# Optimization experiments

Measured on AMD Instinct MI355X. Metric: run time of the kernel, lower is better.

The kernel has to match this reference:

```python
import jax, jax.numpy as jnp
import numpy as np

HEADS = 4
C = 128            # per-head out channels (hard-coded 128 in the module)
NEG_SLOPE_ATT = 0.2   # GATConv attention leaky_relu slope
NEG_SLOPE = 0.01      # F.leaky_relu default slope


def _diag_output_ids(num_groups, n):
    # ids = base_i + n*j + j for group i, agent j; base_i = i * n^2
    i = np.arange(num_groups)[:, None] * (n * n)
    j = np.arange(n)[None, :] * (n + 1)
    return jnp.asarray((i + j).reshape(-1))


def setup_inputs() -> dict:
    key = jax.random.key(0)
    ks = jax.random.split(key, 12)
    num_groups, n_agents = 12, 48
    N = num_groups * n_agents * n_agents      # 27648 nodes
    E = 442368
    F_in, edge_dim, hidden = 256, 16, 256
    s = 0.05
    return {
        "x": jax.random.normal(ks[0], (N, F_in), jnp.float32),
        "edge_index": jax.random.randint(ks[1], (2, E), 0, N, jnp.int32),
        "edge_attr": jax.random.normal(ks[2], (E, edge_dim), jnp.float32),
        "num_groups": num_groups,
        "agents_per_group": n_agents,
        "W": jax.random.normal(ks[3], (F_in, HEADS * C), jnp.float32) * s,
        "att_src": jax.random.normal(ks[4], (HEADS, C), jnp.float32) * s,
        "att_dst": jax.random.normal(ks[5], (HEADS, C), jnp.float32) * s,
        "W_edge": jax.random.normal(ks[6], (edge_dim, HEADS * C), jnp.float32) * s,
        "att_edge": jax.random.normal(ks[7], (HEADS, C), jnp.float32) * s,
        "bias_gat": jnp.zeros((HEADS * C,), jnp.float32),
        "fc_W": jax.random.normal(ks[8], (HEADS * C, hidden), jnp.float32) * s,
        "fc_b": jnp.zeros((hidden,), jnp.float32),
    }


def _gat_conv(x, src, dst, edge_attr_full, W, att_src, att_dst, W_edge, att_edge, bias):
    N = x.shape[0]
    h = (x @ W).reshape(N, HEADS, C)                       # [N,H,C]
    a_src = jnp.einsum('nhc,hc->nh', h, att_src)           # [N,H]
    a_dst = jnp.einsum('nhc,hc->nh', h, att_dst)
    he = (edge_attr_full @ W_edge).reshape(-1, HEADS, C)   # [E',H,C]
    a_edge = jnp.einsum('ehc,hc->eh', he, att_edge)
    logits = jax.nn.leaky_relu(a_src[src] + a_dst[dst] + a_edge, NEG_SLOPE_ATT)
    # segment softmax over incoming edges of each dst node
    m = jax.ops.segment_max(logits, dst, num_segments=N)   # [N,H]
    e = jnp.exp(logits - m[dst])
    s = jax.ops.segment_sum(e, dst, num_segments=N)
    alpha = e / (s[dst] + 1e-16)                           # [E',H]
    msg = h[src] * alpha[..., None]                        # [E',H,C]
    out = jax.ops.segment_sum(msg, dst, num_segments=N)    # [N,H,C]
    return out.reshape(N, HEADS * C) + bias


def reference(x, edge_index, edge_attr, num_groups, agents_per_group,
              W, att_src, att_dst, W_edge, att_edge, bias_gat, fc_W, fc_b):
    N = x.shape[0]
    # add self-loops (PyG default), self-loop edge_attr = mean fill
    loops = jnp.arange(N, dtype=edge_index.dtype)
    src = jnp.concatenate([edge_index[0], loops])
    dst = jnp.concatenate([edge_index[1], loops])
    ea = jnp.concatenate([edge_attr,
                          jnp.broadcast_to(edge_attr.mean(0), (N, edge_attr.shape[1]))])
    h = jax.nn.leaky_relu(
        _gat_conv(x, src, dst, ea, W, att_src, att_dst, W_edge, att_edge, bias_gat),
        NEG_SLOPE)
    ids = _diag_output_ids(num_groups, agents_per_group)
    # fc_output + leaky_relu then diagonal index-select (select first: same math)
    return jax.nn.leaky_relu(h[ids] @ fc_W + fc_b, NEG_SLOPE)
```

## Files before the change

### kernel.cpp

```cpp
#include <hip/hip_runtime.h>

#define NNODES 27648
#define NEDGES 442368
#define FIN    256
#define HC     512
#define NH     4
#define CDIM   128
#define NAG    48
#define NGRP   12
#define N2     2304
#define NOUT   576
#define CAP    128
#define EDIM   16
#define MPART  512


__device__ __forceinline__ float lrelu(float v, float s){ return v > 0.0f ? v : s * v; }

__device__ __forceinline__ float wsum(float v){
  #pragma unroll
  for (int off = 32; off; off >>= 1) v += __shfl_xor(v, off, 64);
  return v;
}
__device__ __forceinline__ float wmax(float v){
  #pragma unroll
  for (int off = 32; off; off >>= 1) v = fmaxf(v, __shfl_xor(v, off, 64));
  return v;
}

__global__ __launch_bounds__(256) void k_pre(
    const float* __restrict__ W, const float* __restrict__ att_src,
    const float* __restrict__ att_dst, const float* __restrict__ W_edge,
    const float* __restrict__ att_edge, const float* __restrict__ ea,
    float* __restrict__ ws_, float* __restrict__ wd_, float* __restrict__ we_,
    int* __restrict__ counts, float4* __restrict__ easum_part){
  int b = blockIdx.x;
  int tid = threadIdx.x;
  if (b < 11) {
    int g = b * 256 + tid;
    if (g < 1024) {
      int f = g >> 2, h = g & 3;
      const float4* wp = (const float4*)(W + f*HC + h*CDIM);
      const float4* ap = (const float4*)(att_src + h*CDIM);
      float s = 0.f;
      #pragma unroll 8
      for (int c4 = 0; c4 < CDIM/4; c4++){
        float4 wv = wp[c4], av = ap[c4];
        s += wv.x*av.x + wv.y*av.y + wv.z*av.z + wv.w*av.w;
      }
      ws_[g] = s;
    } else if (g < 2048) {
      int gg = g - 1024; int f = gg >> 2, h = gg & 3;
      const float4* wp = (const float4*)(W + f*HC + h*CDIM);
      const float4* ap = (const float4*)(att_dst + h*CDIM);
      float s = 0.f;
      #pragma unroll 8
      for (int c4 = 0; c4 < CDIM/4; c4++){
        float4 wv = wp[c4], av = ap[c4];
        s += wv.x*av.x + wv.y*av.y + wv.z*av.z + wv.w*av.w;
      }
      wd_[gg] = s;
    } else if (g < 2112) {
      int gg = g - 2048; int d = gg >> 2, h = gg & 3;
      const float4* wp = (const float4*)(W_edge + d*HC + h*CDIM);
      const float4* ap = (const float4*)(att_edge + h*CDIM);
      float s = 0.f;
      #pragma unroll 8
      for (int c4 = 0; c4 < CDIM/4; c4++){
        float4 wv = wp[c4], av = ap[c4];
        s += wv.x*av.x + wv.y*av.y + wv.z*av.z + wv.w*av.w;
      }
      we_[gg] = s;
    } else if (g < 2112 + NOUT) {
      counts[g - 2112] = 0;
    }
  } else {
    int pb = b - 11;
    const float4* p = (const float4*)ea;
    const int total = NEDGES * 4;
    float4 acc = make_float4(0.f, 0.f, 0.f, 0.f);
    for (int i = pb*256 + tid; i < total; i += MPART*256){
      float4 v = p[i];
      acc.x += v.x; acc.y += v.y; acc.z += v.z; acc.w += v.w;
    }
    #pragma unroll
    for (int off = 4; off <= 32; off <<= 1){
      acc.x += __shfl_xor(acc.x, off, 64);
      acc.y += __shfl_xor(acc.y, off, 64);
      acc.z += __shfl_xor(acc.z, off, 64);
      acc.w += __shfl_xor(acc.w, off, 64);
    }
    __shared__ float4 sd4[16];
    int lane = tid & 63, wave = tid >> 6;
    if (lane < 4) sd4[wave*4 + lane] = acc;
    __syncthreads();
    if (tid < 4){
      float4 t = sd4[tid];
      float4 a = sd4[4+tid], c = sd4[8+tid], d = sd4[12+tid];
      t.x += a.x + c.x + d.x; t.y += a.y + c.y + d.y;
      t.z += a.z + c.z + d.z; t.w += a.w + c.w + d.w;
      easum_part[pb*4 + tid] = t;
    }
  }
}

__global__ __launch_bounds__(256) void k_scan(const int* __restrict__ ei,
    const float* __restrict__ ea, const float* __restrict__ we_,
    int* __restrict__ counts, int* __restrict__ slist, float* __restrict__ aed,
    const float* __restrict__ easum_part, float* __restrict__ easum){
  int tid = threadIdx.x;
  if (blockIdx.x == NEDGES/256){
    int col = tid & 15, part = tid >> 4;
    float s = 0.f;
    for (int pb = 0; pb < MPART/16; pb++)
      s += easum_part[(part*(MPART/16) + pb)*16 + col];
    __shared__ float sd[256];
    sd[tid] = s;
    __syncthreads();
    if (tid < 16){
      float t = 0.f;
      #pragma unroll
      for (int i = 0; i < 16; i++) t += sd[i*16 + tid];
      easum[tid] = t;
    }
    return;
  }
  int e = blockIdx.x*256 + tid;
  int dst = ei[NEDGES + e];
  int r = dst % N2;
  if (r % 49) return;
  int row = (dst / N2) * NAG + r / 49;
  int pos = atomicAdd(&counts[row], 1);
  if (pos >= CAP) return;
  slist[row*CAP + pos] = ei[e];
  const float* eap = ea + (size_t)e*EDIM;
  float a0=0.f,a1=0.f,a2=0.f,a3=0.f;
  #pragma unroll
  for (int d = 0; d < EDIM; d++){
    float v = eap[d];
    a0 += v*we_[d*4+0]; a1 += v*we_[d*4+1]; a2 += v*we_[d*4+2]; a3 += v*we_[d*4+3];
  }
  float* ap = aed + (size_t)(row*CAP+pos)*4;
  ap[0]=a0; ap[1]=a1; ap[2]=a2; ap[3]=a3;
}

__global__ __launch_bounds__(256) void k_mega(const float* __restrict__ x,
    const float* __restrict__ ws_, const float* __restrict__ wd_,
    const float* __restrict__ we_, const float* __restrict__ easum,
    const int* __restrict__ counts, const int* __restrict__ slist,
    const float* __restrict__ aed,
    const float* __restrict__ W, const float* __restrict__ bias,
    const float* __restrict__ fcW, const float* __restrict__ fcb,
    float* __restrict__ out){
  __shared__ float  lg[(CAP+1)*4];
  __shared__ int    srcs[CAP+1];
  __shared__ float  adst_s[4];
  __shared__ float4 pz4[4*256];
  __shared__ float4 zs4[256];
  __shared__ float4 ph4[256];
  __shared__ float  hs[512];
  __shared__ float4 pq4[256];
  int row = blockIdx.x;
  int g = row / NAG, j = row - g*NAG;
  int dst = g*N2 + j*49;
  int tid = threadIdx.x;
  int lane = tid & 63, wave = tid >> 6;
  int k = counts[row]; if (k > CAP) k = CAP;

  float wsr[4][4];
  #pragma unroll
  for (int q = 0; q < 4; q++){
    float4 t = *(const float4*)(ws_ + (lane*4+q)*4);
    wsr[q][0]=t.x; wsr[q][1]=t.y; wsr[q][2]=t.z; wsr[q][3]=t.w;
  }

  for (int i = wave; i < k; i += 4){
    int src = slist[row*CAP + i];
    float4 aedv = *(const float4*)(aed + (size_t)(row*CAP+i)*4);
    float4 xv = *(const float4*)(x + (size_t)src*FIN + lane*4);
    float p0 = xv.x*wsr[0][0] + xv.y*wsr[1][0] + xv.z*wsr[2][0] + xv.w*wsr[3][0];
    float p1 = xv.x*wsr[0][1] + xv.y*wsr[1][1] + xv.z*wsr[2][1] + xv.w*wsr[3][1];
    float p2 = xv.x*wsr[0][2] + xv.y*wsr[1][2] + xv.z*wsr[2][2] + xv.w*wsr[3][2];
    float p3 = xv.x*wsr[0][3] + xv.y*wsr[1][3] + xv.z*wsr[2][3] + xv.w*wsr[3][3];
    p0 = wsum(p0); p1 = wsum(p1); p2 = wsum(p2); p3 = wsum(p3);
    if (lane == 0){
      srcs[i] = src;
      lg[i*4+0] = p0 + aedv.x; lg[i*4+1] = p1 + aedv.y;
      lg[i*4+2] = p2 + aedv.z; lg[i*4+3] = p3 + aedv.w;
    }
  }

  if (wave == 0){
    float wdr[4][4];
    #pragma unroll
    for (int q = 0; q < 4; q++){
      float4 t = *(const float4*)(wd_ + (lane*4+q)*4);
      wdr[q][0]=t.x; wdr[q][1]=t.y; wdr[q][2]=t.z; wdr[q][3]=t.w;
    }
    float4 xv = *(const float4*)(x + (size_t)dst*FIN + lane*4);
    float pd[4], ps[4];
    #pragma unroll
    for (int h = 0; h < 4; h++){
      pd[h] = xv.x*wdr[0][h] + xv.y*wdr[1][h] + xv.z*wdr[2][h] + xv.w*wdr[3][h];
      ps[h] = xv.x*wsr[0][h] + xv.y*wsr[1][h] + xv.z*wsr[2][h] + xv.w*wsr[3][h];
    }
    const float invE = 1.0f/(float)NEDGES;
    float md = (lane < 16) ? easum[lane]*invE : 0.f;
    float al[4];
    #pragma unroll
    for (int h = 0; h < 4; h++){
      float c = (lane < 16) ? md*we_[lane*4+h] : 0.f;
      al[h] = wsum(c);
      pd[h] = wsum(pd[h]);
      ps[h] = wsum(ps[h]);
    }
    if (lane == 0){
      #pragma unroll
      for (int h = 0; h < 4; h++){
        adst_s[h] = pd[h];
        lg[k*4+h] = ps[h] + al[h];
      }
      srcs[k] = dst;
    }
  }
  __syncthreads();

  {
    int h = wave;
    float ad = adst_s[h];
    float m = -1e30f;
    for (int i = lane; i <= k; i += 64){
      float v = lrelu(lg[i*4+h] + ad, 0.2f);
      lg[i*4+h] = v;
      m = fmaxf(m, v);
    }
    m = wmax(m);
    float s = 0.f;
    for (int i = lane; i <= k; i += 64){
      float e = __expf(lg[i*4+h] - m);
      lg[i*4+h] = e;
      s += e;
    }
    s = wsum(s);
    float inv = 1.0f/(s + 1e-16f);
    for (int i = lane; i <= k; i += 64) lg[i*4+h] *= inv;
  }
  __syncthreads();

  {
    float acc[4][4];
    #pragma unroll
    for (int h = 0; h < 4; h++)
      #pragma unroll
      for (int c = 0; c < 4; c++) acc[h][c] = 0.f;
    for (int i = wave; i <= k; i += 4){
      int src = srcs[i];
      float4 xv = *(const float4*)(x + (size_t)src*FIN + lane*4);
      float a0 = lg[i*4+0], a1 = lg[i*4+1], a2 = lg[i*4+2], a3 = lg[i*4+3];
      acc[0][0] += a0*xv.x; acc[0][1] += a0*xv.y; acc[0][2] += a0*xv.z; acc[0][3] += a0*xv.w;
      acc[1][0] += a1*xv.x; acc[1][1] += a1*xv.y; acc[1][2] += a1*xv.z; acc[1][3] += a1*xv.w;
      acc[2][0] += a2*xv.x; acc[2][1] += a2*xv.y; acc[2][2] += a2*xv.z; acc[2][3] += a2*xv.w;
      acc[3][0] += a3*xv.x; acc[3][1] += a3*xv.y; acc[3][2] += a3*xv.z; acc[3][3] += a3*xv.w;
    }
    #pragma unroll
    for (int h = 0; h < 4; h++)
      pz4[wave*256 + h*64 + lane] =
        make_float4(acc[h][0], acc[h][1], acc[h][2], acc[h][3]);
  }
  __syncthreads();
  {
    float4 a = pz4[0*256+tid], b = pz4[1*256+tid],
           c = pz4[2*256+tid], d = pz4[3*256+tid];
    zs4[tid] = make_float4(a.x+b.x+c.x+d.x, a.y+b.y+c.y+d.y,
                           a.z+b.z+c.z+d.z, a.w+b.w+c.w+d.w);
  }
  __syncthreads();

  {
    int cg = tid & 127;
    int half = tid >> 7;
    int h = cg >> 5;
    const float* zp = (const float*)zs4 + h*256 + half*128;
    const float4* Wp = (const float4*)(W + (size_t)half*128*HC) + cg;
    float4 acc = make_float4(0.f,0.f,0.f,0.f);
    #pragma unroll 8
    for (int r = 0; r < 128; r++){
      float4 w4 = Wp[(size_t)r*(HC/4)];
      float zv = zp[r];
      acc.x += zv*w4.x; acc.y += zv*w4.y; acc.z += zv*w4.z; acc.w += zv*w4.w;
    }
    ph4[half*128 + cg] = acc;
  }
  __syncthreads();
  if (tid < 128){
    float4 a = ph4[tid], b = ph4[128+tid];
    float4 bs = *(const float4*)(bias + 4*tid);
    hs[4*tid+0] = lrelu(a.x+b.x+bs.x, 0.01f);
    hs[4*tid+1] = lrelu(a.y+b.y+bs.y, 0.01f);
    hs[4*tid+2] = lrelu(a.z+b.z+bs.z, 0.01f);
    hs[4*tid+3] = lrelu(a.w+b.w+bs.w, 0.01f);
  }
  __syncthreads();

  {
    int cg = tid & 63;
    int q  = tid >> 6;
    const float4* Fp = (const float4*)(fcW + (size_t)q*128*256) + cg;
    const float* hp = hs + q*128;
    float4 acc = make_float4(0.f,0.f,0.f,0.f);
    #pragma unroll 8
    for (int r = 0; r < 128; r++){
      float4 w4 = Fp[(size_t)r*64];
      float hv = hp[r];
      acc.x += hv*w4.x; acc.y += hv*w4.y; acc.z += hv*w4.z; acc.w += hv*w4.w;
    }
    pq4[q*64 + cg] = acc;
  }
  __syncthreads();
  if (tid < 64){
    float4 a = pq4[tid],      b = pq4[64+tid];
    float4 c = pq4[128+tid],  d = pq4[192+tid];
    float4 bs = *(const float4*)(fcb + 4*tid);
    float4 o;
    o.x = lrelu(a.x+b.x+c.x+d.x+bs.x, 0.01f);
    o.y = lrelu(a.y+b.y+c.y+d.y+bs.y, 0.01f);
    o.z = lrelu(a.z+b.z+c.z+d.z+bs.z, 0.01f);
    o.w = lrelu(a.w+b.w+c.w+d.w+bs.w, 0.01f);
    *(float4*)(out + (size_t)row*256 + 4*tid) = o;
  }
}

extern "C" void kernel_launch(void* const* d_in, const int* in_sizes, int n_in,
                              void* d_out, int out_size, void* d_ws, size_t ws_size,
                              hipStream_t stream) {
  const float* x        = (const float*)d_in[0];
  const int*   ei       = (const int*)  d_in[1];
  const float* ea       = (const float*)d_in[2];
  const float* W        = (const float*)d_in[5];
  const float* att_src  = (const float*)d_in[6];
  const float* att_dst  = (const float*)d_in[7];
  const float* W_edge   = (const float*)d_in[8];
  const float* att_edge = (const float*)d_in[9];
  const float* bias     = (const float*)d_in[10];
  const float* fcW      = (const float*)d_in[11];
  const float* fcb      = (const float*)d_in[12];
  float* out = (float*)d_out;

  float* w = (float*)d_ws;
  float*  ws_       = w;
  float*  wd_       = w + 1024;
  float*  we_       = w + 2048;
  float*  easum     = w + 2112;
  int*    counts    = (int*)(w + 2128);
  float*  easum_p   = w + 2704;
  int*    slist     = (int*)(w + 10896);
  float*  aed       = w + 84624;

  k_pre<<<11 + MPART, 256, 0, stream>>>(W, att_src, att_dst, W_edge, att_edge, ea,
                                        ws_, wd_, we_, counts, (float4*)easum_p);
  k_scan<<<NEDGES/256 + 1, 256, 0, stream>>>(ei, ea, we_, counts, slist, aed,
                                             easum_p, easum);
  k_mega<<<NOUT, 256, 0, stream>>>(x, ws_, wd_, we_, easum, counts, slist, aed,
                                   W, bias, fcW, fcb, out);
}
```

Before: 156.6 us.

## Process two output rows per block to share W and fc weight loads

k_mega now handles two destination rows per 512-thread block, with each group of four waves doing gather and softmax for one row. The two dense projections (W and fc_W) are split over more K-slices, and each weight load feeds both rows' accumulators, which halves the global weight traffic per row. The cost is half as many blocks (288), which may underfill the GPU, plus larger shared memory use and an extra reduction step.

```diff
diff --git a/kernel.cpp b/kernel.cpp
--- a/kernel.cpp
+++ b/kernel.cpp
@@ -144,7 +144,7 @@
   ap[0]=a0; ap[1]=a1; ap[2]=a2; ap[3]=a3;
 }
 
-__global__ __launch_bounds__(256) void k_mega(const float* __restrict__ x,
+__global__ __launch_bounds__(512) void k_mega(const float* __restrict__ x,
     const float* __restrict__ ws_, const float* __restrict__ wd_,
     const float* __restrict__ we_, const float* __restrict__ easum,
     const int* __restrict__ counts, const int* __restrict__ slist,
@@ -152,20 +152,24 @@
     const float* __restrict__ W, const float* __restrict__ bias,
     const float* __restrict__ fcW, const float* __restrict__ fcb,
     float* __restrict__ out){
-  __shared__ float  lg[(CAP+1)*4];
-  __shared__ int    srcs[CAP+1];
-  __shared__ float  adst_s[4];
-  __shared__ float4 pz4[4*256];
-  __shared__ float4 zs4[256];
-  __shared__ float4 ph4[256];
-  __shared__ float  hs[512];
-  __shared__ float4 pq4[256];
-  int row = blockIdx.x;
-  int g = row / NAG, j = row - g*NAG;
-  int dst = g*N2 + j*49;
+  __shared__ float  lg[2][(CAP+1)*4];
+  __shared__ int    srcs[2][CAP+1];
+  __shared__ float  adst[2][4];
+  __shared__ float4 zs4[2][256];
+  __shared__ float  hsf[2][512];
+  __shared__ float4 scratch[2048];
+  int rowA = blockIdx.x * 2;
   int tid = threadIdx.x;
   int lane = tid & 63, wave = tid >> 6;
-  int k = counts[row]; if (k > CAP) k = CAP;
+  int rsel = wave >> 2;
+  int w4 = wave & 3;
+
+  int kA = counts[rowA];     if (kA > CAP) kA = CAP;
+  int kB = counts[rowA + 1]; if (kB > CAP) kB = CAP;
+  int myRow = rowA + rsel;
+  int myK = rsel ? kB : kA;
+  int gg = myRow / NAG, jj = myRow - gg*NAG;
+  int myDst = gg*N2 + jj*49;
 
   float wsr[4][4];
   #pragma unroll
@@ -174,9 +178,9 @@
     wsr[q][0]=t.x; wsr[q][1]=t.y; wsr[q][2]=t.z; wsr[q][3]=t.w;
   }
 
-  for (int i = wave; i < k; i += 4){
-    int src = slist[row*CAP + i];
-    float4 aedv = *(const float4*)(aed + (size_t)(row*CAP+i)*4);
+  for (int i = w4; i < myK; i += 4){
+    int src = slist[myRow*CAP + i];
+    float4 aedv = *(const float4*)(aed + (size_t)(myRow*CAP+i)*4);
     float4 xv = *(const float4*)(x + (size_t)src*FIN + lane*4);
     float p0 = xv.x*wsr[0][0] + xv.y*wsr[1][0] + xv.z*wsr[2][0] + xv.w*wsr[3][0];
     float p1 = xv.x*wsr[0][1] + xv.y*wsr[1][1] + xv.z*wsr[2][1] + xv.w*wsr[3][1];
@@ -184,20 +188,20 @@
     float p3 = xv.x*wsr[0][3] + xv.y*wsr[1][3] + xv.z*wsr[2][3] + xv.w*wsr[3][3];
     p0 = wsum(p0); p1 = wsum(p1); p2 = wsum(p2); p3 = wsum(p3);
     if (lane == 0){
-      srcs[i] = src;
-      lg[i*4+0] = p0 + aedv.x; lg[i*4+1] = p1 + aedv.y;
-      lg[i*4+2] = p2 + aedv.z; lg[i*4+3] = p3 + aedv.w;
-    }
-  }
-
-  if (wave == 0){
+      srcs[rsel][i] = src;
+      lg[rsel][i*4+0] = p0 + aedv.x; lg[rsel][i*4+1] = p1 + aedv.y;
+      lg[rsel][i*4+2] = p2 + aedv.z; lg[rsel][i*4+3] = p3 + aedv.w;
+    }
+  }
+
+  if (w4 == 0){
     float wdr[4][4];
     #pragma unroll
     for (int q = 0; q < 4; q++){
       float4 t = *(const float4*)(wd_ + (lane*4+q)*4);
       wdr[q][0]=t.x; wdr[q][1]=t.y; wdr[q][2]=t.z; wdr[q][3]=t.w;
     }
-    float4 xv = *(const float4*)(x + (size_t)dst*FIN + lane*4);
+    float4 xv = *(const float4*)(x + (size_t)myDst*FIN + lane*4);
     float pd[4], ps[4];
     #pragma unroll
     for (int h = 0; h < 4; h++){
@@ -217,33 +221,34 @@
     if (lane == 0){
       #pragma unroll
       for (int h = 0; h < 4; h++){
-        adst_s[h] = pd[h];
-        lg[k*4+h] = ps[h] + al[h];
+        adst[rsel][h] = pd[h];
+        lg[rsel][myK*4+h] = ps[h] + al[h];
       }
-      srcs[k] = dst;
-    }
-  }
-  __syncthreads();
-
-  {
-    int h = wave;
-    float ad = adst_s[h];
+      srcs[rsel][myK] = myDst;
+    }
+  }
+  __syncthreads();
+
+  {
+    int r = wave >> 2, h = wave & 3;
+    int kk = r ? kB : kA;
+    float ad = adst[r][h];
     float m = -1e30f;
-    for (int i = lane; i <= k; i += 64){
-      float v = lrelu(lg[i*4+h] + ad, 0.2f);
-      lg[i*4+h] = v;
+    for (int i = lane; i <= kk; i += 64){
+      float v = lrelu(lg[r][i*4+h] + ad, 0.2f);
+      lg[r][i*4+h] = v;
       m = fmaxf(m, v);
     }
     m = wmax(m);
     float s = 0.f;
-    for (int i = lane; i <= k; i += 64){
-      float e = __expf(lg[i*4+h] - m);
-      lg[i*4+h] = e;
+    for (int i = lane; i <= kk; i += 64){
+      float e = __expf(lg[r][i*4+h] - m);
+      lg[r][i*4+h] = e;
       s += e;
     }
     s = wsum(s);
     float inv = 1.0f/(s + 1e-16f);
-    for (int i = lane; i <= k; i += 64) lg[i*4+h] *= inv;
+    for (int i = lane; i <= kk; i += 64) lg[r][i*4+h] *= inv;
   }
   __syncthreads();
 
@@ -253,10 +258,11 @@
     for (int h = 0; h < 4; h++)
       #pragma unroll
       for (int c = 0; c < 4; c++) acc[h][c] = 0.f;
-    for (int i = wave; i <= k; i += 4){
-      int src = srcs[i];
+    for (int i = w4; i <= myK; i += 4){
+      int src = srcs[rsel][i];
       float4 xv = *(const float4*)(x + (size_t)src*FIN + lane*4);
-      float a0 = lg[i*4+0], a1 = lg[i*4+1], a2 = lg[i*4+2], a3 = lg[i*4+3];
+      float a0 = lg[rsel][i*4+0], a1 = lg[rsel][i*4+1];
+      float a2 = lg[rsel][i*4+2], a3 = lg[rsel][i*4+3];
       acc[0][0] += a0*xv.x; acc[0][1] += a0*xv.y; acc[0][2] += a0*xv.z; acc[0][3] += a0*xv.w;
       acc[1][0] += a1*xv.x; acc[1][1] += a1*xv.y; acc[1][2] += a1*xv.z; acc[1][3] += a1*xv.w;
       acc[2][0] += a2*xv.x; acc[2][1] += a2*xv.y; acc[2][2] += a2*xv.z; acc[2][3] += a2*xv.w;
@@ -264,69 +270,85 @@
     }
     #pragma unroll
     for (int h = 0; h < 4; h++)
-      pz4[wave*256 + h*64 + lane] =
+      scratch[rsel*1024 + w4*256 + h*64 + lane] =
         make_float4(acc[h][0], acc[h][1], acc[h][2], acc[h][3]);
   }
   __syncthreads();
   {
-    float4 a = pz4[0*256+tid], b = pz4[1*256+tid],
-           c = pz4[2*256+tid], d = pz4[3*256+tid];
-    zs4[tid] = make_float4(a.x+b.x+c.x+d.x, a.y+b.y+c.y+d.y,
-                           a.z+b.z+c.z+d.z, a.w+b.w+c.w+d.w);
+    int r = tid >> 8, s = tid & 255;
+    float4 a = scratch[r*1024 + 0*256 + s], b = scratch[r*1024 + 1*256 + s];
+    float4 c = scratch[r*1024 + 2*256 + s], d = scratch[r*1024 + 3*256 + s];
+    zs4[r][s] = make_float4(a.x+b.x+c.x+d.x, a.y+b.y+c.y+d.y,
+                            a.z+b.z+c.z+d.z, a.w+b.w+c.w+d.w);
   }
   __syncthreads();
 
   {
     int cg = tid & 127;
-    int half = tid >> 7;
-    int h = cg >> 5;
-    const float* zp = (const float*)zs4 + h*256 + half*128;
-    const float4* Wp = (const float4*)(W + (size_t)half*128*HC) + cg;
-    float4 acc = make_float4(0.f,0.f,0.f,0.f);
+    int q  = tid >> 7;
+    int h  = cg >> 5;
+    const float* zA = (const float*)&zs4[0][0] + h*256 + q*64;
+    const float* zB = (const float*)&zs4[1][0] + h*256 + q*64;
+    const float4* Wp = (const float4*)(W + (size_t)q*64*HC) + cg;
+    float4 aA = make_float4(0.f,0.f,0.f,0.f);
+    float4 aB = make_float4(0.f,0.f,0.f,0.f);
     #pragma unroll 8
-    for (int r = 0; r < 128; r++){
-      float4 w4 = Wp[(size_t)r*(HC/4)];
-      float zv = zp[r];
-      acc.x += zv*w4.x; acc.y += zv*w4.y; acc.z += zv*w4.z; acc.w += zv*w4.w;
-    }
-    ph4[half*128 + cg] = acc;
+    for (int r = 0; r < 64; r++){
+      float4 w4v = Wp[(size_t)r*(HC/4)];
+      float za = zA[r], zb = zB[r];
+      aA.x += za*w4v.x; aA.y += za*w4v.y; aA.z += za*w4v.z; aA.w += za*w4v.w;
+      aB.x += zb*w4v.x; aB.y += zb*w4v.y; aB.z += zb*w4v.z; aB.w += zb*w4v.w;
+    }
+    scratch[0*512 + q*128 + cg] = aA;
+    scratch[1*512 + q*128 + cg] = aB;
+  }
+  __syncthreads();
+  if (tid < 256){
+    int r = tid >> 7, cg = tid & 127;
+    float4 a = scratch[r*512 + 0*128 + cg], b = scratch[r*512 + 1*128 + cg];
+    float4 c = scratch[r*512 + 2*128 + cg], d = scratch[r*512 + 3*128 + cg];
+    float4 bs = ((const float4*)bias)[cg];
+    hsf[r][4*cg+0] = lrelu(a.x+b.x+c.x+d.x+bs.x, 0.01f);
+    hsf[r][4*cg+1] = lrelu(a.y+b.y+c.y+d.y+bs.y, 0.01f);
+    hsf[r][4*cg+2] = lrelu(a.z+b.z+c.z+d.z+bs.z, 0.01f);
+    hsf[r][4*cg+3] = lrelu(a.w+b.w+c.w+d.w+bs.w, 0.01f);
+  }
+  __syncthreads();
+
+  {
+    int cg = tid & 63;
+    int e  = tid >> 6;
+    const float4* Fp = (const float4*)(fcW + (size_t)e*64*256) + cg;
+    const float* hA = &hsf[0][0] + e*64;
+    const float* hB = &hsf[1][0] + e*64;
+    float4 aA = make_float4(0.f,0.f,0.f,0.f);
+    float4 aB = make_float4(0.f,0.f,0.f,0.f);
+    #pragma unroll 8
+    for (int r = 0; r < 64; r++){
+      float4 w4v = Fp[(size_t)r*64];
+      float ha = hA[r], hb = hB[r];
+      aA.x += ha*w4v.x; aA.y += ha*w4v.y; aA.z += ha*w4v.z; aA.w += ha*w4v.w;
+      aB.x += hb*w4v.x; aB.y += hb*w4v.y; aB.z += hb*w4v.z; aB.w += hb*w4v.w;
+    }
+    scratch[0*512 + e*64 + cg] = aA;
+    scratch[1*512 + e*64 + cg] = aB;
   }
   __syncthreads();
   if (tid < 128){
-    float4 a = ph4[tid], b = ph4[128+tid];
-    float4 bs = *(const float4*)(bias + 4*tid);
-    hs[4*tid+0] = lrelu(a.x+b.x+bs.x, 0.01f);
-    hs[4*tid+1] = lrelu(a.y+b.y+bs.y, 0.01f);
-    hs[4*tid+2] = lrelu(a.z+b.z+bs.z, 0.01f);
-    hs[4*tid+3] = lrelu(a.w+b.w+bs.w, 0.01f);
-  }
-  __syncthreads();
-
-  {
-    int cg = tid & 63;
-    int q  = tid >> 6;
-    const float4* Fp = (const float4*)(fcW + (size_t)q*128*256) + cg;
-    const float* hp = hs + q*128;
-    float4 acc = make_float4(0.f,0.f,0.f,0.f);
-    #pragma unroll 8
-    for (int r = 0; r < 128; r++){
-      float4 w4 = Fp[(size_t)r*64];
-      float hv = hp[r];
-      acc.x += hv*w4.x; acc.y += hv*w4.y; acc.z += hv*w4.z; acc.w += hv*w4.w;
-    }
-    pq4[q*64 + cg] = acc;
-  }
-  __syncthreads();
-  if (tid < 64){
-    float4 a = pq4[tid],      b = pq4[64+tid];
-    float4 c = pq4[128+tid],  d = pq4[192+tid];
-    float4 bs = *(const float4*)(fcb + 4*tid);
+    int r = tid >> 6, cg = tid & 63;
+    float4 s0 = scratch[r*512 + 0*64 + cg];
+    #pragma unroll
+    for (int e = 1; e < 8; e++){
+      float4 t = scratch[r*512 + e*64 + cg];
+      s0.x += t.x; s0.y += t.y; s0.z += t.z; s0.w += t.w;
+    }
+    float4 bs = ((const float4*)fcb)[cg];
     float4 o;
-    o.x = lrelu(a.x+b.x+c.x+d.x+bs.x, 0.01f);
-    o.y = lrelu(a.y+b.y+c.y+d.y+bs.y, 0.01f);
-    o.z = lrelu(a.z+b.z+c.z+d.z+bs.z, 0.01f);
-    o.w = lrelu(a.w+b.w+c.w+d.w+bs.w, 0.01f);
-    *(float4*)(out + (size_t)row*256 + 4*tid) = o;
+    o.x = lrelu(s0.x+bs.x, 0.01f);
+    o.y = lrelu(s0.y+bs.y, 0.01f);
+    o.z = lrelu(s0.z+bs.z, 0.01f);
+    o.w = lrelu(s0.w+bs.w, 0.01f);
+    *(float4*)(out + (size_t)(rowA + r)*256 + 4*cg) = o;
   }
 }
 
@@ -360,6 +382,6 @@
                                         ws_, wd_, we_, counts, (float4*)easum_p);
   k_scan<<<NEDGES/256 + 1, 256, 0, stream>>>(ei, ea, we_, counts, slist, aed,
                                              easum_p, easum);
-  k_mega<<<NOUT, 256, 0, stream>>>(x, ws_, wd_, we_, easum, counts, slist, aed,
-                                   W, bias, fcW, fcb, out);
-}
+  k_mega<<<NOUT/2, 512, 0, stream>>>(x, ws_, wd_, we_, easum, counts, slist, aed,
+                                     W, bias, fcW, fcb, out);
+}
```

Result: faster. 149.6 us (-4.5%).
